# Performance work log

Measured on AMD Instinct MI355X. Metric: run time of the kernel, lower is better.

## Reference

```python
import jax, jax.numpy as jnp
import numpy as np

K = 3          # involution kernel size
GROUPS = 32    # channels == GROUPS * K*K
BN_EPS = 1e-5

def _conv1x1(x, W, b):
    # x: (B,C,H,W), W: (Co,C), b: (Co,)
    return jnp.einsum('bchw,oc->bohw', x, W) + b[None, :, None, None]

def setup_inputs() -> dict:
    key = jax.random.key(0)
    ks = jax.random.split(key, 5)
    C = GROUPS * K * K  # 288
    x = jax.random.normal(ks[0], (8, C, 64, 64), dtype=jnp.float32)
    Wi = jax.random.normal(ks[1], (C, C), dtype=jnp.float32) * 0.05
    bi = jnp.zeros((C,), dtype=jnp.float32)
    gamma = jnp.ones((C,), dtype=jnp.float32)
    beta = jnp.zeros((C,), dtype=jnp.float32)
    Wo = jax.random.normal(ks[2], (C, C), dtype=jnp.float32) * 0.05
    bo = jnp.zeros((C,), dtype=jnp.float32)
    return {"x": x, "Wi": Wi, "bi": bi, "gamma": gamma, "beta": beta, "Wo": Wo, "bo": bo}

def reference(x, Wi, bi, gamma, beta, Wo, bo):
    B, C, H, W = x.shape
    # kernel generation branch (stride=1 -> avgpool is identity)
    tmp = jax.nn.relu(_conv1x1(x, Wi, bi))
    # BatchNorm2d in training mode: batch stats over (N,H,W), biased variance
    mean = jnp.mean(tmp, axis=(0, 2, 3), keepdims=True)
    var = jnp.var(tmp, axis=(0, 2, 3), keepdims=True)
    tmp = (tmp - mean) * jax.lax.rsqrt(var + BN_EPS)
    tmp = tmp * gamma[None, :, None, None] + beta[None, :, None, None]
    ker = _conv1x1(tmp, Wo, bo)                       # (B, G*K^2, H, W)
    ker = ker.reshape(B, GROUPS, K * K, H, W)         # (B, G, K^2, H, W)
    # unfold: extract KxK patches with padding (K-1)//2, stride 1
    p = (K - 1) // 2
    xp = jnp.pad(x, ((0, 0), (0, 0), (p, p), (p, p)))
    patches = jnp.stack(
        [xp[:, :, i:i + H, j:j + W] for i in range(K) for j in range(K)],
        axis=2,
    )  # (B, C, K^2, H, W), kernel-position minor — matches torch unfold layout
    patches = patches.reshape(B, GROUPS, C // GROUPS, K * K, H, W)
    # per-pixel dynamic kernel multiply + sum over kernel positions
    out = jnp.einsum('bgkhw,bgckhw->bgchw', ker, patches)
    return out.reshape(B, C, H, W)
```

## Files before the change

### kernel.cpp

```cpp
#include <hip/hip_runtime.h>

#define CH   288
#define GRPS 32
#define CPG  9
#define IMH  64
#define IMW  64
#define HW   4096
#define NB   8
#define NPX  (NB * HW)
#define BN_EPS 1e-5f

typedef short bf16x8 __attribute__((ext_vector_type(8)));
typedef float f32x4  __attribute__((ext_vector_type(4)));

#define XT_OFF   0u
#define WIB_OFF  18874368u
#define WOS_OFF  19040256u
#define S1_OFF   19206144u
#define S2_OFF   19207296u
#define SC_OFF   19208448u
#define SH_OFF   19209600u
#define BO2_OFF  19210752u

#define BUFB 20480

__device__ __forceinline__ unsigned short f2b(float f) {
    unsigned int u = __float_as_uint(f);
    return (unsigned short)((u + 0x7fffu + ((u >> 16) & 1u)) >> 16);
}
__device__ __forceinline__ float b2f(unsigned short h) {
    return __uint_as_float(((unsigned int)h) << 16);
}

#define GLDS(g, l) __builtin_amdgcn_global_load_lds( \
    (const __attribute__((address_space(1))) void*)(g), \
    (__attribute__((address_space(3))) void*)(l), 16, 0, 0)

__device__ __forceinline__ f32x4 mfma16(bf16x8 a, bf16x8 b, f32x4 c) {
    return __builtin_amdgcn_mfma_f32_16x16x32_bf16(a, b, c, 0, 0, 0);
}

#define TS 40
__global__ __launch_bounds__(256) void k_transpose(const float* __restrict__ x,
                                                   unsigned short* __restrict__ xt) {
    __shared__ unsigned short T[64 * TS];
    const int tid = threadIdx.x;
    const int p0 = blockIdx.x * 64;
    const int c0 = blockIdx.y * 32;
    const int b  = blockIdx.z;
    #pragma unroll
    for (int it = 0; it < 2; ++it) {
        const int item  = it * 256 + tid;
        const int c_loc = item >> 4;
        const int p4    = item & 15;
        const float4 v = *(const float4*)(x + (size_t)(b * CH + c0 + c_loc) * HW + p0 + p4 * 4);
        const int px = p4 * 4;
        T[(px + 0) * TS + c_loc] = f2b(v.x);
        T[(px + 1) * TS + c_loc] = f2b(v.y);
        T[(px + 2) * TS + c_loc] = f2b(v.z);
        T[(px + 3) * TS + c_loc] = f2b(v.w);
    }
    __syncthreads();
    const int px_loc = tid >> 2;
    const int cq     = tid & 3;
    const uint4 o = *(const uint4*)((const char*)T + px_loc * (TS * 2) + cq * 16);
    *(uint4*)(xt + ((size_t)b * HW + p0 + px_loc) * CH + c0 + cq * 8) = o;
}

__global__ __launch_bounds__(256) void k_cvt_wi(const float* __restrict__ Wi,
                                                unsigned short* __restrict__ Wib) {
    const int idx = blockIdx.x * 256 + threadIdx.x;
    const float4 v = ((const float4*)Wi)[idx];
    unsigned short h[4] = {f2b(v.x), f2b(v.y), f2b(v.z), f2b(v.w)};
    *(uint2*)(Wib + (size_t)idx * 4) = *(const uint2*)h;
}

#define STAGE2(XSRC, WSRC, K0v, DST) do {                                      \
    for (int s = wave; s < 20; s += 4) {                                       \
        const int row = s * 16 + lrow;                             \
        const int sc  = lp ^ ((row >> 1) & 3);                                 \
        const unsigned short* g = (s < 2)                                      \
            ? (XSRC) + (size_t)row * CH + (K0v) + sc * 8                       \
            : (WSRC) + (size_t)(row - 32) * CH + (K0v) + sc * 8;               \
        GLDS(g, (DST) + s * 1024);                                             \
    }                                                                          \
} while (0)

#define GSTEP(BUF) do {                                                        \
    const int xr = pxh * 16 + r;                                               \
    const bf16x8 xf = *(const bf16x8*)((BUF) + xr * 64 +                       \
                         ((q ^ ((xr >> 1) & 3)) * 16));                        \
    _Pragma("unroll")                                                          \
    for (int j = 0; j < 9; ++j) {                                              \
        const int wr = 32 + chh * 144 + j * 16 + r;                            \
        const bf16x8 wf = *(const bf16x8*)((BUF) + wr * 64 +                   \
                             ((q ^ ((wr >> 1) & 3)) * 16));                    \
        acc[j] = mfma16(wf, xf, acc[j]);                                       \
    }                                                                          \
} while (0)

#define KLOOP(XSRC, WSRC) do {                                                 \
    STAGE2(XSRC, WSRC, 0, smc);                                                \
    asm volatile("s_waitcnt vmcnt(0)" ::: "memory");                           \
    __builtin_amdgcn_s_barrier();                                              \
    _Pragma("unroll 1")                                                        \
    for (int kk = 0; kk < 8; ++kk) {                                           \
        STAGE2(XSRC, WSRC, (kk + 1) * 32, smc + ((kk + 1) & 1) * BUFB);        \
        asm volatile("s_waitcnt vmcnt(5)" ::: "memory");                       \
        __builtin_amdgcn_s_barrier();                                          \
        GSTEP(smc + (kk & 1) * BUFB);                                          \
        __builtin_amdgcn_s_barrier();                                          \
    }                                                                          \
    asm volatile("s_waitcnt vmcnt(0)" ::: "memory");                           \
    __builtin_amdgcn_s_barrier();                                              \
    GSTEP(smc);                                                                \
} while (0)

__global__ __launch_bounds__(256, 4) void k_gemm1(const unsigned short* __restrict__ Wib,
                                                  const float* __restrict__ bi,
                                                  unsigned short* __restrict__ xt,
                                                  float* __restrict__ s1g) {
    __shared__ char smc[2 * BUFB];

    const int tid  = threadIdx.x;
    const int wave = tid >> 6;
    const int lane = tid & 63;
    const int q    = lane >> 4;
    const int r    = lane & 15;
    const int pxh  = wave & 1;
    const int chh  = wave >> 1;
    const int p0   = blockIdx.x * 32;
    const int lrow = lane >> 4 == 0 ? lane >> 2 : lane >> 2;
    const int lrow2 = lane >> 2;
    const int lp   = lane & 3;
    (void)lrow;
    #define lrow lrow2

    f32x4 acc[9];
    #pragma unroll
    for (int j = 0; j < 9; ++j) acc[j] = (f32x4)0.0f;

    KLOOP(xt + (size_t)p0 * CH, Wib);
    __syncthreads();

    float* sstat = (float*)(smc + 38656);
    for (int c2 = tid; c2 < 576; c2 += 256) sstat[c2] = 0.0f;
    __syncthreads();

    #pragma unroll 1
    for (int j = 0; j < 9; ++j) {
        const int cb = chh * 144 + j * 16 + q * 4;
        const float4 b4 = *(const float4*)(bi + cb);
        float v[4];
        v[0] = fmaxf(acc[j][0] + b4.x, 0.0f);
        v[1] = fmaxf(acc[j][1] + b4.y, 0.0f);
        v[2] = fmaxf(acc[j][2] + b4.z, 0.0f);
        v[3] = fmaxf(acc[j][3] + b4.w, 0.0f);
        unsigned short h[4] = {f2b(v[0]), f2b(v[1]), f2b(v[2]), f2b(v[3])};
        *(uint2*)(smc + (pxh * 16 + r) * 576 + cb * 2) = *(const uint2*)h;
        float a1[4] = {v[0], v[1], v[2], v[3]};
        float a2[4] = {v[0]*v[0], v[1]*v[1], v[2]*v[2], v[3]*v[3]};
        #pragma unroll
        for (int m = 1; m < 16; m <<= 1) {
            #pragma unroll
            for (int i = 0; i < 4; ++i) {
                a1[i] += __shfl_xor(a1[i], m, 64);
                a2[i] += __shfl_xor(a2[i], m, 64);
            }
        }
        if (r == 0) {
            #pragma unroll
            for (int i = 0; i < 4; ++i) {
                atomicAdd(&sstat[cb + i], a1[i]);
                atomicAdd(&sstat[288 + cb + i], a2[i]);
            }
        }
    }
    __syncthreads();

    for (int idx = tid; idx < 1152; idx += 256) {
        const int row = idx / 36;
        const int off = idx - row * 36;
        *(uint4*)(xt + (size_t)(p0 + row) * CH + off * 8) =
            *(const uint4*)(smc + row * 576 + off * 16);
    }
    for (int c2 = tid; c2 < 576; c2 += 256)
        atomicAdd(&s1g[c2], sstat[c2]);
    #undef lrow
}

__global__ __launch_bounds__(320) void k_scale(const float* __restrict__ s1,
                                               const float* __restrict__ s2,
                                               const float* __restrict__ gamma,
                                               const float* __restrict__ beta,
                                               float* __restrict__ scale,
                                               float* __restrict__ shift) {
    const int c = threadIdx.x;
    if (c < CH) {
        const float inv = 1.0f / (float)(NB * HW);
        const float mean = s1[c] * inv;
        const float var  = s2[c] * inv - mean * mean;
        const float rs   = rsqrtf(var + BN_EPS);
        const float sc   = gamma[c] * rs;
        scale[c] = sc;
        shift[c] = beta[c] - mean * sc;
    }
}

__global__ __launch_bounds__(64) void k_fold(const float* __restrict__ Wo,
                                             const float* __restrict__ bo,
                                             const float* __restrict__ scale,
                                             const float* __restrict__ shift,
                                             unsigned short* __restrict__ Wos,
                                             float* __restrict__ bo2) {
    const int m = blockIdx.x;
    const int t = threadIdx.x;
    float s = 0.0f;
    for (int k = t; k < CH; k += 64) {
        const float wv = Wo[(size_t)m * CH + k];
        s += wv * shift[k];
        Wos[(size_t)m * CH + k] = f2b(wv * scale[k]);
    }
    #pragma unroll
    for (int off = 32; off > 0; off >>= 1) s += __shfl_down(s, off, 64);
    if (t == 0) bo2[m] = bo[m] + s;
}

#define KLS 36
__global__ __launch_bounds__(256, 4) void k_gemm2_invol(const unsigned short* __restrict__ xt,
                                                        const unsigned short* __restrict__ Wos,
                                                        const float* __restrict__ bo2,
                                                        const float* __restrict__ x,
                                                        float* __restrict__ out) {
    __shared__ char smc[2 * BUFB];
    unsigned short* kerL = (unsigned short*)smc;

    const int tid  = threadIdx.x;
    const int wave = tid >> 6;
    const int lane = tid & 63;
    const int q    = lane >> 4;
    const int r    = lane & 15;
    const int pxh  = wave & 1;
    const int chh  = wave >> 1;
    const int p0   = blockIdx.x * 32;
    const int b    = blockIdx.y;
    const int h    = p0 >> 6;
    const int w0   = p0 & 63;
    const size_t rowbase = (size_t)b * HW + p0;
    const int lrow = lane >> 2;
    const int lp   = lane & 3;

    f32x4 acc[9];
    #pragma unroll
    for (int j = 0; j < 9; ++j) acc[j] = (f32x4)0.0f;

    KLOOP(xt + rowbase * CH, Wos);
    __syncthreads();

    const int pxl = pxh * 16 + r;
    #pragma unroll
    for (int j = 0; j < 9; ++j) {
        const int cb = chh * 144 + j * 16 + q * 4;
        const float4 bz = *(const float4*)(bo2 + cb);
        kerL[(cb + 0) * KLS + pxl] = f2b(acc[j][0] + bz.x);
        kerL[(cb + 1) * KLS + pxl] = f2b(acc[j][1] + bz.y);
        kerL[(cb + 2) * KLS + pxl] = f2b(acc[j][2] + bz.z);
        kerL[(cb + 3) * KLS + pxl] = f2b(acc[j][3] + bz.w);
    }
    __syncthreads();

    const int tm = tid >> 3;
    const int tn = tid & 7;
    const int wb = w0 + tn * 4;
    #pragma unroll 1
    for (int i = 0; i < 9; ++i) {
        const int ch = tm + 32 * i;
        const int cb = (ch / CPG) * CPG;
        float xv[3][6];
        #pragma unroll
        for (int dr = 0; dr < 3; ++dr) {
            const int hh = h + dr - 1;
            const bool rv = (hh >= 0) && (hh < IMH);
            const float* xr2 = x + ((size_t)(b * CH + ch) * IMH + (rv ? hh : 0)) * IMW;
            if (rv) {
                const float4 m4 = *(const float4*)(xr2 + wb);
                xv[dr][1] = m4.x; xv[dr][2] = m4.y; xv[dr][3] = m4.z; xv[dr][4] = m4.w;
                xv[dr][0] = (wb > 0)       ? xr2[wb - 1] : 0.0f;
                xv[dr][5] = (wb + 4 < IMW) ? xr2[wb + 4] : 0.0f;
            } else {
                #pragma unroll
                for (int j = 0; j < 6; ++j) xv[dr][j] = 0.0f;
            }
        }
        float o[4] = {0.0f, 0.0f, 0.0f, 0.0f};
        #pragma unroll
        for (int k = 0; k < 9; ++k) {
            const int dr = k / 3, dc = k % 3;
            const uint2 kk = *(const uint2*)(kerL + (cb + k) * KLS + tn * 4);
            const unsigned short* ks = (const unsigned short*)&kk;
            #pragma unroll
            for (int j = 0; j < 4; ++j)
                o[j] += b2f(ks[j]) * xv[dr][j + dc];
        }
        float4 ov = {o[0], o[1], o[2], o[3]};
        *(float4*)(out + ((size_t)(b * CH + ch) * IMH + h) * IMW + wb) = ov;
    }
}

extern "C" void kernel_launch(void* const* d_in, const int* in_sizes, int n_in,
                              void* d_out, int out_size, void* d_ws, size_t ws_size,
                              hipStream_t stream) {
    const float* x     = (const float*)d_in[0];
    const float* Wi    = (const float*)d_in[1];
    const float* bi    = (const float*)d_in[2];
    const float* gamma = (const float*)d_in[3];
    const float* beta  = (const float*)d_in[4];
    const float* Wo    = (const float*)d_in[5];
    const float* bo    = (const float*)d_in[6];
    float* out = (float*)d_out;

    char* ws = (char*)d_ws;
    unsigned short* xt  = (unsigned short*)(ws + XT_OFF);
    unsigned short* Wib = (unsigned short*)(ws + WIB_OFF);
    unsigned short* Wos = (unsigned short*)(ws + WOS_OFF);
    float* s1    = (float*)(ws + S1_OFF);
    float* s2    = (float*)(ws + S2_OFF);
    float* scale = (float*)(ws + SC_OFF);
    float* shift = (float*)(ws + SH_OFF);
    float* bo2   = (float*)(ws + BO2_OFF);

    k_transpose<<<dim3(HW / 64, CH / 32, NB), 256, 0, stream>>>(x, xt);
    k_cvt_wi<<<dim3(CH * CH / 1024), 256, 0, stream>>>(Wi, Wib);
    hipMemsetAsync(ws + S1_OFF, 0, 2 * CH * sizeof(float), stream);
    k_gemm1<<<dim3(NPX / 32), 256, 0, stream>>>(Wib, bi, xt, s1);
    k_scale<<<dim3(1), 320, 0, stream>>>(s1, s2, gamma, beta, scale, shift);
    k_fold<<<dim3(CH), 64, 0, stream>>>(Wo, bo, scale, shift, Wos, bo2);
    k_gemm2_invol<<<dim3(HW / 32, NB), 256, 0, stream>>>(xt, Wos, bo2, x, out);
}
```

Measured before the change: 204.1 us.

## Pre-swizzle weights into MFMA fragment layout and load directly from global

Weights Wi and folded Wo are written into an MFMA-fragment-ordered layout, so each lane reads its weight fragment straight from global/L2 instead of staging through LDS. Only the 32-pixel activation tile is staged into LDS, in one shot, which removes the double-buffered k-loop and its barriers. The Wi conversion and the stats zeroing are folded into the transpose kernel, which saves a launch and a memset. BN statistics now go to 64 slots to reduce atomic contention, and the scale kernel reduces over the slots. The trade-off is that weight reads now depend on cache hits, and the whole K tile of the activations must sit in LDS.

Result: faster. 198.6 us (-2.7%).

```diff
diff --git a/kernel.cpp b/kernel.cpp
--- a/kernel.cpp
+++ b/kernel.cpp
@@ -9,6 +9,7 @@
 #define NB   8
 #define NPX  (NB * HW)
 #define BN_EPS 1e-5f
+#define NSLOT 64
 
 typedef short bf16x8 __attribute__((ext_vector_type(8)));
 typedef float f32x4  __attribute__((ext_vector_type(4)));
@@ -16,13 +17,10 @@
 #define XT_OFF   0u
 #define WIB_OFF  18874368u
 #define WOS_OFF  19040256u
-#define S1_OFF   19206144u
-#define S2_OFF   19207296u
 #define SC_OFF   19208448u
 #define SH_OFF   19209600u
 #define BO2_OFF  19210752u
 
-#define BUFB 20480
 
 __device__ __forceinline__ unsigned short f2b(float f) {
     unsigned int u = __float_as_uint(f);
@@ -40,14 +38,53 @@
     return __builtin_amdgcn_mfma_f32_16x16x32_bf16(a, b, c, 0, 0, 0);
 }
 
+#define STAGE_X32(XSRC) do {                                                   \
+    for (int s = wave; s < 18; s += 4) {                                       \
+        const int d   = s * 1024 + lane * 16;                                  \
+        const int px  = d / 576;                                               \
+        const int rem = d - px * 576;                                          \
+        const int kc  = rem >> 6;                                              \
+        const int ch  = (rem >> 4) & 3;                                        \
+        const int sc  = ch ^ ((px >> 1) & 3);                                  \
+        GLDS((XSRC) + (size_t)px * CH + kc * 32 + sc * 8, smc + s * 1024);     \
+    }                                                                          \
+} while (0)
+
 #define TS 40
-__global__ __launch_bounds__(256) void k_transpose(const float* __restrict__ x,
-                                                   unsigned short* __restrict__ xt) {
+__global__ __launch_bounds__(256) void k_pre(const float* __restrict__ x,
+                                             unsigned short* __restrict__ xt,
+                                             const float* __restrict__ Wi,
+                                             unsigned short* __restrict__ WibF,
+                                             float* __restrict__ slots) {
     __shared__ unsigned short T[64 * TS];
     const int tid = threadIdx.x;
     const int p0 = blockIdx.x * 64;
     const int c0 = blockIdx.y * 32;
     const int b  = blockIdx.z;
+
+    if (blockIdx.z == 0) {
+        if (blockIdx.y == 0) {
+            for (int i = blockIdx.x * 256 + tid; i < NSLOT * 576; i += 64 * 256)
+                slots[i] = 0.0f;
+        } else if (blockIdx.y == 1) {
+            for (int id = blockIdx.x * 256 + tid; id < 162 * 64; id += 64 * 256) {
+                const int t    = id >> 6;
+                const int lane = id & 63;
+                const int q    = lane >> 4;
+                const int r    = lane & 15;
+                const int jt   = t / 9;
+                const int kk   = t - jt * 9;
+                const int row  = jt * 16 + r;
+                const int k0   = kk * 32 + q * 8;
+                const float4 a = *(const float4*)(Wi + (size_t)row * CH + k0);
+                const float4 bq = *(const float4*)(Wi + (size_t)row * CH + k0 + 4);
+                unsigned short h[8] = {f2b(a.x), f2b(a.y), f2b(a.z), f2b(a.w),
+                                       f2b(bq.x), f2b(bq.y), f2b(bq.z), f2b(bq.w)};
+                *(uint4*)(WibF + (size_t)t * 512 + lane * 8) = *(const uint4*)h;
+            }
+        }
+    }
+
     #pragma unroll
     for (int it = 0; it < 2; ++it) {
         const int item  = it * 256 + tid;
@@ -67,60 +104,11 @@
     *(uint4*)(xt + ((size_t)b * HW + p0 + px_loc) * CH + c0 + cq * 8) = o;
 }
 
-__global__ __launch_bounds__(256) void k_cvt_wi(const float* __restrict__ Wi,
-                                                unsigned short* __restrict__ Wib) {
-    const int idx = blockIdx.x * 256 + threadIdx.x;
-    const float4 v = ((const float4*)Wi)[idx];
-    unsigned short h[4] = {f2b(v.x), f2b(v.y), f2b(v.z), f2b(v.w)};
-    *(uint2*)(Wib + (size_t)idx * 4) = *(const uint2*)h;
-}
-
-#define STAGE2(XSRC, WSRC, K0v, DST) do {                                      \
-    for (int s = wave; s < 20; s += 4) {                                       \
-        const int row = s * 16 + lrow;                             \
-        const int sc  = lp ^ ((row >> 1) & 3);                                 \
-        const unsigned short* g = (s < 2)                                      \
-            ? (XSRC) + (size_t)row * CH + (K0v) + sc * 8                       \
-            : (WSRC) + (size_t)(row - 32) * CH + (K0v) + sc * 8;               \
-        GLDS(g, (DST) + s * 1024);                                             \
-    }                                                                          \
-} while (0)
-
-#define GSTEP(BUF) do {                                                        \
-    const int xr = pxh * 16 + r;                                               \
-    const bf16x8 xf = *(const bf16x8*)((BUF) + xr * 64 +                       \
-                         ((q ^ ((xr >> 1) & 3)) * 16));                        \
-    _Pragma("unroll")                                                          \
-    for (int j = 0; j < 9; ++j) {                                              \
-        const int wr = 32 + chh * 144 + j * 16 + r;                            \
-        const bf16x8 wf = *(const bf16x8*)((BUF) + wr * 64 +                   \
-                             ((q ^ ((wr >> 1) & 3)) * 16));                    \
-        acc[j] = mfma16(wf, xf, acc[j]);                                       \
-    }                                                                          \
-} while (0)
-
-#define KLOOP(XSRC, WSRC) do {                                                 \
-    STAGE2(XSRC, WSRC, 0, smc);                                                \
-    asm volatile("s_waitcnt vmcnt(0)" ::: "memory");                           \
-    __builtin_amdgcn_s_barrier();                                              \
-    _Pragma("unroll 1")                                                        \
-    for (int kk = 0; kk < 8; ++kk) {                                           \
-        STAGE2(XSRC, WSRC, (kk + 1) * 32, smc + ((kk + 1) & 1) * BUFB);        \
-        asm volatile("s_waitcnt vmcnt(5)" ::: "memory");                       \
-        __builtin_amdgcn_s_barrier();                                          \
-        GSTEP(smc + (kk & 1) * BUFB);                                          \
-        __builtin_amdgcn_s_barrier();                                          \
-    }                                                                          \
-    asm volatile("s_waitcnt vmcnt(0)" ::: "memory");                           \
-    __builtin_amdgcn_s_barrier();                                              \
-    GSTEP(smc);                                                                \
-} while (0)
-
-__global__ __launch_bounds__(256, 4) void k_gemm1(const unsigned short* __restrict__ Wib,
-                                                  const float* __restrict__ bi,
-                                                  unsigned short* __restrict__ xt,
-                                                  float* __restrict__ s1g) {
-    __shared__ char smc[2 * BUFB];
+__global__ __launch_bounds__(256) void k_gemm1(const unsigned short* __restrict__ WibF,
+                                               const float* __restrict__ bi,
+                                               unsigned short* __restrict__ xt,
+                                               float* __restrict__ slots) {
+    __shared__ char smc[20736];
 
     const int tid  = threadIdx.x;
     const int wave = tid >> 6;
@@ -130,20 +118,30 @@
     const int pxh  = wave & 1;
     const int chh  = wave >> 1;
     const int p0   = blockIdx.x * 32;
-    const int lrow = lane >> 4 == 0 ? lane >> 2 : lane >> 2;
-    const int lrow2 = lane >> 2;
-    const int lp   = lane & 3;
-    (void)lrow;
-    #define lrow lrow2
 
     f32x4 acc[9];
     #pragma unroll
     for (int j = 0; j < 9; ++j) acc[j] = (f32x4)0.0f;
 
-    KLOOP(xt + (size_t)p0 * CH, Wib);
-    __syncthreads();
-
-    float* sstat = (float*)(smc + 38656);
+    STAGE_X32(xt + (size_t)p0 * CH);
+    asm volatile("s_waitcnt vmcnt(0)" ::: "memory");
+    __syncthreads();
+
+    #pragma unroll
+    for (int kk = 0; kk < 9; ++kk) {
+        const int xr = pxh * 16 + r;
+        const bf16x8 xf = *(const bf16x8*)(smc + xr * 576 + kk * 64 +
+                                           ((q ^ ((xr >> 1) & 3)) * 16));
+        #pragma unroll
+        for (int j = 0; j < 9; ++j) {
+            const bf16x8 wf = *(const bf16x8*)(WibF +
+                (size_t)((chh * 9 + j) * 9 + kk) * 512 + lane * 8);
+            acc[j] = mfma16(wf, xf, acc[j]);
+        }
+    }
+    __syncthreads();
+
+    float* sstat = (float*)(smc + 18432);
     for (int c2 = tid; c2 < 576; c2 += 256) sstat[c2] = 0.0f;
     __syncthreads();
 
@@ -184,26 +182,31 @@
         *(uint4*)(xt + (size_t)(p0 + row) * CH + off * 8) =
             *(const uint4*)(smc + row * 576 + off * 16);
     }
+    float* slot = slots + (size_t)(blockIdx.x & (NSLOT - 1)) * 576;
     for (int c2 = tid; c2 < 576; c2 += 256)
-        atomicAdd(&s1g[c2], sstat[c2]);
-    #undef lrow
-}
-
-__global__ __launch_bounds__(320) void k_scale(const float* __restrict__ s1,
-                                               const float* __restrict__ s2,
+        atomicAdd(&slot[c2], sstat[c2]);
+}
+
+__global__ __launch_bounds__(576) void k_scale(const float* __restrict__ slots,
                                                const float* __restrict__ gamma,
                                                const float* __restrict__ beta,
                                                float* __restrict__ scale,
                                                float* __restrict__ shift) {
-    const int c = threadIdx.x;
-    if (c < CH) {
-        const float inv = 1.0f / (float)(NB * HW);
-        const float mean = s1[c] * inv;
-        const float var  = s2[c] * inv - mean * mean;
+    __shared__ float red[576];
+    const int tid = threadIdx.x;
+    float s = 0.0f;
+    #pragma unroll 4
+    for (int sl = 0; sl < NSLOT; ++sl) s += slots[sl * 576 + tid];
+    red[tid] = s;
+    __syncthreads();
+    if (tid < CH) {
+        const float inv  = 1.0f / (float)(NB * HW);
+        const float mean = red[tid] * inv;
+        const float var  = red[288 + tid] * inv - mean * mean;
         const float rs   = rsqrtf(var + BN_EPS);
-        const float sc   = gamma[c] * rs;
-        scale[c] = sc;
-        shift[c] = beta[c] - mean * sc;
+        const float sc   = gamma[tid] * rs;
+        scale[tid] = sc;
+        shift[tid] = beta[tid] - mean * sc;
     }
 }
 
@@ -211,28 +214,38 @@
                                              const float* __restrict__ bo,
                                              const float* __restrict__ scale,
                                              const float* __restrict__ shift,
-                                             unsigned short* __restrict__ Wos,
+                                             unsigned short* __restrict__ WosF,
                                              float* __restrict__ bo2) {
     const int m = blockIdx.x;
     const int t = threadIdx.x;
     float s = 0.0f;
-    for (int k = t; k < CH; k += 64) {
-        const float wv = Wo[(size_t)m * CH + k];
-        s += wv * shift[k];
-        Wos[(size_t)m * CH + k] = f2b(wv * scale[k]);
-    }
+    for (int k = t; k < CH; k += 64) s += Wo[(size_t)m * CH + k] * shift[k];
     #pragma unroll
     for (int off = 32; off > 0; off >>= 1) s += __shfl_down(s, off, 64);
     if (t == 0) bo2[m] = bo[m] + s;
+
+    if (t < 36) {
+        const int kk = t >> 2;
+        const int q  = t & 3;
+        const int jt = m >> 4;
+        const int rr = m & 15;
+        const int k0 = kk * 32 + q * 8;
+        unsigned short h[8];
+        #pragma unroll
+        for (int j = 0; j < 8; ++j)
+            h[j] = f2b(Wo[(size_t)m * CH + k0 + j] * scale[k0 + j]);
+        *(uint4*)(WosF + (size_t)(jt * 9 + kk) * 512 + (q * 16 + rr) * 8) =
+            *(const uint4*)h;
+    }
 }
 
 #define KLS 36
-__global__ __launch_bounds__(256, 4) void k_gemm2_invol(const unsigned short* __restrict__ xt,
-                                                        const unsigned short* __restrict__ Wos,
-                                                        const float* __restrict__ bo2,
-                                                        const float* __restrict__ x,
-                                                        float* __restrict__ out) {
-    __shared__ char smc[2 * BUFB];
+__global__ __launch_bounds__(256) void k_gemm2_invol(const unsigned short* __restrict__ xt,
+                                                     const unsigned short* __restrict__ WosF,
+                                                     const float* __restrict__ bo2,
+                                                     const float* __restrict__ x,
+                                                     float* __restrict__ out) {
+    __shared__ char smc[20736];
     unsigned short* kerL = (unsigned short*)smc;
 
     const int tid  = threadIdx.x;
@@ -247,14 +260,27 @@
     const int h    = p0 >> 6;
     const int w0   = p0 & 63;
     const size_t rowbase = (size_t)b * HW + p0;
-    const int lrow = lane >> 2;
-    const int lp   = lane & 3;
 
     f32x4 acc[9];
     #pragma unroll
     for (int j = 0; j < 9; ++j) acc[j] = (f32x4)0.0f;
 
-    KLOOP(xt + rowbase * CH, Wos);
+    STAGE_X32(xt + rowbase * CH);
+    asm volatile("s_waitcnt vmcnt(0)" ::: "memory");
+    __syncthreads();
+
+    #pragma unroll
+    for (int kk = 0; kk < 9; ++kk) {
+        const int xr = pxh * 16 + r;
+        const bf16x8 xf = *(const bf16x8*)(smc + xr * 576 + kk * 64 +
+                                           ((q ^ ((xr >> 1) & 3)) * 16));
+        #pragma unroll
+        for (int j = 0; j < 9; ++j) {
+            const bf16x8 wf = *(const bf16x8*)(WosF +
+                (size_t)((chh * 9 + j) * 9 + kk) * 512 + lane * 8);
+            acc[j] = mfma16(wf, xf, acc[j]);
+        }
+    }
     __syncthreads();
 
     const int pxl = pxh * 16 + r;
@@ -320,20 +346,17 @@
     float* out = (float*)d_out;
 
     char* ws = (char*)d_ws;
-    unsigned short* xt  = (unsigned short*)(ws + XT_OFF);
-    unsigned short* Wib = (unsigned short*)(ws + WIB_OFF);
-    unsigned short* Wos = (unsigned short*)(ws + WOS_OFF);
-    float* s1    = (float*)(ws + S1_OFF);
-    float* s2    = (float*)(ws + S2_OFF);
+    unsigned short* xt   = (unsigned short*)(ws + XT_OFF);
+    unsigned short* WibF = (unsigned short*)(ws + WIB_OFF);
+    unsigned short* WosF = (unsigned short*)(ws + WOS_OFF);
+    float* slots = (float*)(ws + WOS_OFF);
     float* scale = (float*)(ws + SC_OFF);
     float* shift = (float*)(ws + SH_OFF);
     float* bo2   = (float*)(ws + BO2_OFF);
 
-    k_transpose<<<dim3(HW / 64, CH / 32, NB), 256, 0, stream>>>(x, xt);
-    k_cvt_wi<<<dim3(CH * CH / 1024), 256, 0, stream>>>(Wi, Wib);
-    hipMemsetAsync(ws + S1_OFF, 0, 2 * CH * sizeof(float), stream);
-    k_gemm1<<<dim3(NPX / 32), 256, 0, stream>>>(Wib, bi, xt, s1);
-    k_scale<<<dim3(1), 320, 0, stream>>>(s1, s2, gamma, beta, scale, shift);
-    k_fold<<<dim3(CH), 64, 0, stream>>>(Wo, bo, scale, shift, Wos, bo2);
-    k_gemm2_invol<<<dim3(HW / 32, NB), 256, 0, stream>>>(xt, Wos, bo2, x, out);
-}
+    k_pre<<<dim3(HW / 64, CH / 32, NB), 256, 0, stream>>>(x, xt, Wi, WibF, slots);
+    k_gemm1<<<dim3(NPX / 32), 256, 0, stream>>>(WibF, bi, xt, slots);
+    k_scale<<<dim3(1), 576, 0, stream>>>(slots, gamma, beta, scale, shift);
+    k_fold<<<dim3(CH), 64, 0, stream>>>(Wo, bo, scale, shift, WosF, bo2);
+    k_gemm2_invol<<<dim3(HW / 32, NB), 256, 0, stream>>>(xt, WosF, bo2, x, out);
+}
```
